# Kernel tuning notes

Measured on AMD Instinct MI355X. Metric: run time of the kernel, lower is better.

The kernel has to match this reference:

```python
import jax, jax.numpy as jnp
import numpy as np

H, HKV, DH = 32, 8, 128
ROPE_BASE = 500000.0


def _rope(x, pos):
    # x: [B, H, T, D]; MLX non-traditional rope (split halves)
    D = x.shape[-1]
    half = D // 2
    freqs = ROPE_BASE ** (-(jnp.arange(half, dtype=jnp.float32) * 2.0 / D))  # [half]
    t = pos + jnp.arange(x.shape[2], dtype=jnp.float32)                      # [T]
    ang = t[:, None] * freqs[None, :]                                        # [T, half]
    cos, sin = jnp.cos(ang), jnp.sin(ang)
    x1, x2 = x[..., :half], x[..., half:]
    return jnp.concatenate([x1 * cos - x2 * sin, x1 * sin + x2 * cos], axis=-1)


def setup_inputs() -> dict:
    key = jax.random.key(0)
    ks = jax.random.split(key, 5)
    B, T, HID = 1, 2048, 4096
    s = 0.02
    return {
        "hidden_states": jax.random.normal(ks[0], (B, T, HID), jnp.float32),
        "Wq": jax.random.normal(ks[1], (H * DH, HID), jnp.float32) * s,
        "Wk": jax.random.normal(ks[2], (HKV * DH, HID), jnp.float32) * s,
        "Wv": jax.random.normal(ks[3], (HKV * DH, HID), jnp.float32) * s,
        "Wo": jax.random.normal(ks[4], (HID, H * DH), jnp.float32) * s,
        "k_cache": jnp.zeros((1, HKV, 4096, DH), jnp.float32),
        "v_cache": jnp.zeros((1, HKV, 4096, DH), jnp.float32),
        "pos_int": 0,
    }


def reference(hidden_states, Wq, Wk, Wv, Wo, k_cache, v_cache, pos_int):
    B, T, _ = hidden_states.shape
    # QKV projections (no bias, Llama-style) -> [B, h, T, D]
    q = (hidden_states @ Wq.T).reshape(B, T, H, DH).transpose(0, 2, 1, 3)
    k = (hidden_states @ Wk.T).reshape(B, T, HKV, DH).transpose(0, 2, 1, 3)
    v = (hidden_states @ Wv.T).reshape(B, T, HKV, DH).transpose(0, 2, 1, 3)
    # RoPE with position offset
    q = _rope(q, pos_int)
    k = _rope(k, pos_int)
    # KV-cache scatter update at pos_int, then window to [:pos_int+T]
    k_cache = jax.lax.dynamic_update_slice(k_cache, k, (0, 0, pos_int, 0))
    v_cache = jax.lax.dynamic_update_slice(v_cache, v, (0, 0, pos_int, 0))
    Tk = pos_int + T
    k_win = k_cache[:, :, :Tk, :]
    v_win = v_cache[:, :, :Tk, :]
    # GQA: repeat_interleave KV heads to match query heads
    group = H // HKV
    k_ = jnp.repeat(k_win, group, axis=1)   # [B, H, Tk, D]
    v_ = jnp.repeat(v_win, group, axis=1)
    # SDPA, is_causal=True => top-left aligned causal mask (query i sees keys j<=i)
    scale = 1.0 / jnp.sqrt(jnp.asarray(DH, jnp.float32))
    scores = jnp.einsum("bhtd,bhsd->bhts", q, k_) * scale  # [B, H, T, Tk]
    causal = jnp.arange(Tk)[None, :] <= jnp.arange(T)[:, None]
    scores = jnp.where(causal[None, None], scores, jnp.finfo(scores.dtype).min)
    attn = jax.nn.softmax(scores, axis=-1)
    out = jnp.einsum("bhts,bhsd->bhtd", attn, v_)           # [B, H, T, D]
    out = out.transpose(0, 2, 1, 3).reshape(B, T, H * DH)
    return out @ Wo.T
```

## Files before the change

kernel.cpp:

```cpp
#include <hip/hip_runtime.h>


#define DEVI __device__ __forceinline__

typedef __attribute__((ext_vector_type(8))) short short8;
typedef __attribute__((ext_vector_type(4))) float f32x4;

DEVI unsigned short f2bf(float f) {
  union { float f; unsigned u; } x; x.f = f;
  unsigned r = x.u + 0x7FFFu + ((x.u >> 16) & 1u);
  return (unsigned short)(r >> 16);
}
DEVI float bf2f(unsigned short h) {
  union { unsigned u; float f; } x; x.u = ((unsigned)h) << 16;
  return x.f;
}
DEVI f32x4 mfma16(short8 a, short8 b, f32x4 c) {
  return __builtin_amdgcn_mfma_f32_16x16x32_bf16(a, b, c, 0, 0, 0);
}
DEVI void gl2lds16(const unsigned short* g, unsigned short* l) {
  __builtin_amdgcn_global_load_lds(
      (const __attribute__((address_space(1))) unsigned int*)g,
      (__attribute__((address_space(3))) unsigned int*)l, 16, 0, 0);
}
DEVI void bar() { __builtin_amdgcn_s_barrier(); }
DEVI void sfence() { __builtin_amdgcn_sched_barrier(0); }

DEVI void cvt_region(const float* __restrict__ src,
                     unsigned short* __restrict__ dst, int n4, int start,
                     int stride) {
  for (int i = start; i < n4; i += stride) {
    float4 v = ((const float4*)src)[i];
    ushort4 h;
    h.x = f2bf(v.x); h.y = f2bf(v.y); h.z = f2bf(v.z); h.w = f2bf(v.w);
    ((ushort4*)dst)[i] = h;
  }
}
__global__ __launch_bounds__(256)
void cvt5_kernel(const float* __restrict__ s0, const float* __restrict__ s1,
                 const float* __restrict__ s2, const float* __restrict__ s3,
                 const float* __restrict__ s4,
                 unsigned short* __restrict__ d0, unsigned short* __restrict__ d1,
                 unsigned short* __restrict__ d2, unsigned short* __restrict__ d3,
                 unsigned short* __restrict__ d4,
                 int n0, int n1, int n2, int n3, int n4) {
  const int start = blockIdx.x * 256 + threadIdx.x;
  const int stride = gridDim.x * 256;
  cvt_region(s0, d0, n0, start, stride);
  cvt_region(s1, d1, n1, start, stride);
  cvt_region(s2, d2, n2, start, stride);
  cvt_region(s3, d3, n3, start, stride);
  cvt_region(s4, d4, n4, start, stride);
}

__global__ __launch_bounds__(512, 2)
void gemm_qkv_8ph(const unsigned short* __restrict__ hsb,
                  const unsigned short* __restrict__ Wqb,
                  const unsigned short* __restrict__ Wkb,
                  const unsigned short* __restrict__ Wvb,
                  unsigned short* __restrict__ Qb,
                  unsigned short* __restrict__ Kb,
                  unsigned short* __restrict__ Vb) {
  const int K = 4096;
  const int NT = 64;
  __shared__ __align__(16) unsigned short Ls[2][2][2][256][32];
  const int tid = threadIdx.x, lane = tid & 63, w = tid >> 6;
  const int wr = w >> 2, wc = w & 3;
  const int bid = blockIdx.x;
  const int m0 = (bid & 7) * 256;
  const int n0g = (bid >> 3) * 256;

  const unsigned short* Bsrc; unsigned short* outp; int ldo, oc;
  if (n0g < 4096)      { Bsrc = Wqb + (size_t)n0g * K;          outp = Qb; ldo = 4096; oc = n0g; }
  else if (n0g < 5120) { Bsrc = Wkb + (size_t)(n0g - 4096) * K; outp = Kb; ldo = 1024; oc = n0g - 4096; }
  else                 { Bsrc = Wvb + (size_t)(n0g - 5120) * K; outp = Vb; ldo = 1024; oc = n0g - 5120; }
  const unsigned short* Asrc = hsb + (size_t)m0 * K;

  auto stageU = [&](const unsigned short* src, int ab, int kh, int tt, int bb) {
#pragma unroll
    for (int j = 0; j < 2; ++j) {
      const int seg = j * 8 + w;
      const int row = seg * 16 + (lane >> 2);
      const int cs  = (lane & 3) ^ ((row >> 1) & 3);
      gl2lds16(src + (size_t)row * K + tt * 64 + kh * 32 + cs * 8,
               &Ls[bb][ab][kh][seg * 16][0]);
    }
  };
  auto ldA = [&](int bb, int kh, int fm) -> short8 {
    const int ra = wr * 128 + fm * 16 + (lane & 15);
    const int cs = (lane >> 4) ^ ((ra >> 1) & 3);
    return *(const short8*)&Ls[bb][0][kh][ra][cs * 8];
  };
  auto ldB = [&](int bb, int kh, int fn) -> short8 {
    const int rb = wc * 64 + fn * 16 + (lane & 15);
    const int cs = (lane >> 4) ^ ((rb >> 1) & 3);
    return *(const short8*)&Ls[bb][1][kh][rb][cs * 8];
  };

  f32x4 acc[8][4];
#pragma unroll
  for (int i = 0; i < 8; ++i)
#pragma unroll
    for (int j = 0; j < 4; ++j) acc[i][j] = (f32x4){0.f, 0.f, 0.f, 0.f};

  stageU(Asrc, 0, 0, 0, 0);
  stageU(Asrc, 0, 1, 0, 0);
  stageU(Bsrc, 1, 0, 0, 0);
  stageU(Bsrc, 1, 1, 0, 0);
  stageU(Bsrc, 1, 0, 1, 1);
  stageU(Asrc, 0, 0, 1, 1);
  stageU(Bsrc, 1, 1, 1, 1);
  asm volatile("s_waitcnt vmcnt(6)" ::: "memory");
  bar();
  sfence();

  short8 af[4], bfr[4];
  for (int t = 0; t < NT; ++t) {
    const int bb = t & 1, nb = bb ^ 1;
#pragma unroll
    for (int i = 0; i < 4; ++i) af[i] = ldA(bb, 0, i);
#pragma unroll
    for (int i = 0; i < 4; ++i) bfr[i] = ldB(bb, 0, i);
    if (t + 1 < NT) stageU(Asrc, 0, 1, t + 1, nb);
    bar();
    __builtin_amdgcn_s_setprio(1);
#pragma unroll
    for (int i = 0; i < 4; ++i)
#pragma unroll
      for (int j = 0; j < 4; ++j) acc[i][j] = mfma16(af[i], bfr[j], acc[i][j]);
    __builtin_amdgcn_s_setprio(0);
    sfence(); bar(); sfence();
#pragma unroll
    for (int i = 0; i < 4; ++i) af[i] = ldA(bb, 0, 4 + i);
    if (t + 2 < NT) stageU(Bsrc, 1, 0, t + 2, bb);
    bar();
    __builtin_amdgcn_s_setprio(1);
#pragma unroll
    for (int i = 0; i < 4; ++i)
#pragma unroll
      for (int j = 0; j < 4; ++j) acc[4 + i][j] = mfma16(af[i], bfr[j], acc[4 + i][j]);
    __builtin_amdgcn_s_setprio(0);
    sfence(); bar(); sfence();
#pragma unroll
    for (int i = 0; i < 4; ++i) af[i] = ldA(bb, 1, i);
#pragma unroll
    for (int i = 0; i < 4; ++i) bfr[i] = ldB(bb, 1, i);
    if (t + 2 < NT) stageU(Asrc, 0, 0, t + 2, bb);
    bar();
    __builtin_amdgcn_s_setprio(1);
#pragma unroll
    for (int i = 0; i < 4; ++i)
#pragma unroll
      for (int j = 0; j < 4; ++j) acc[i][j] = mfma16(af[i], bfr[j], acc[i][j]);
    __builtin_amdgcn_s_setprio(0);
    sfence(); bar(); sfence();
#pragma unroll
    for (int i = 0; i < 4; ++i) af[i] = ldA(bb, 1, 4 + i);
    if (t + 2 < NT) stageU(Bsrc, 1, 1, t + 2, bb);
    bar();
    __builtin_amdgcn_s_setprio(1);
#pragma unroll
    for (int i = 0; i < 4; ++i)
#pragma unroll
      for (int j = 0; j < 4; ++j) acc[4 + i][j] = mfma16(af[i], bfr[j], acc[4 + i][j]);
    __builtin_amdgcn_s_setprio(0);
    if (t < NT - 2) asm volatile("s_waitcnt vmcnt(6)" ::: "memory");
    else            asm volatile("s_waitcnt vmcnt(0)" ::: "memory");
    sfence(); bar(); sfence();
  }

#pragma unroll
  for (int fm = 0; fm < 8; ++fm) {
    const int rb0 = m0 + wr * 128 + fm * 16 + ((lane >> 4) << 2);
#pragma unroll
    for (int fn = 0; fn < 4; ++fn) {
      const int cb = oc + wc * 64 + fn * 16 + (lane & 15);
#pragma unroll
      for (int r = 0; r < 4; ++r)
        outp[(size_t)(rb0 + r) * ldo + cb] = f2bf(acc[fm][fn][r]);
    }
  }
}

__global__ __launch_bounds__(256)
void postproc_kernel(const unsigned short* __restrict__ Vb,
                     unsigned short* __restrict__ VtG,
                     unsigned short* __restrict__ Qb,
                     unsigned short* __restrict__ Kb,
                     const int* __restrict__ posp) {
  __shared__ unsigned short tile[64][68];
  const int b = blockIdx.x, tid = threadIdx.x;
  if (b < 512) {
    const int t0 = (b & 31) * 64;
    const int c0 = (b >> 5) * 64;
    const int r = tid >> 4;
    const int c4 = (tid & 15) << 2;
#pragma unroll
    for (int i = 0; i < 4; ++i) {
      ushort4 v = *(const ushort4*)(Vb + (size_t)(t0 + r + i * 16) * 1024 + c0 + c4);
      *(ushort4*)&tile[r + i * 16][c4] = v;
    }
    __syncthreads();
#pragma unroll
    for (int i = 0; i < 4; ++i) {
      int d = r + i * 16;
      ushort4 o;
      o.x = tile[c4 + 0][d]; o.y = tile[c4 + 1][d];
      o.z = tile[c4 + 2][d]; o.w = tile[c4 + 3][d];
      *(ushort4*)(VtG + (size_t)(c0 + d) * 2048 + t0 + c4) = o;
    }
    return;
  }
  const int QP = 2048 * 32 * 64;
  const int KP = 2048 * 8 * 64;
  int idx = (b - 512) * 256 + tid;
  if (idx >= QP + KP) return;
  unsigned short* base; int t, hh, d, ld;
  if (idx < QP) {
    base = Qb; ld = 4096;
    t = idx >> 11; int rem = idx & 2047; hh = rem >> 6; d = rem & 63;
  } else {
    int j = idx - QP; base = Kb; ld = 1024;
    t = j >> 9; int rem = j & 511; hh = rem >> 6; d = rem & 63;
  }
  float freq = exp2f(-(float)d * 0.29580575880077f);
  float ang = (float)(t + posp[0]) * freq;
  float s, c;
  __sincosf(ang, &s, &c);
  size_t i1 = (size_t)t * ld + hh * 128 + d;
  float x1 = bf2f(base[i1]), x2 = bf2f(base[i1 + 64]);
  base[i1]      = f2bf(x1 * c - x2 * s);
  base[i1 + 64] = f2bf(x1 * s + x2 * c);
}

__global__ __launch_bounds__(512)
void attn_kernel(const unsigned short* __restrict__ Qb,
                 const unsigned short* __restrict__ Kb,
                 const unsigned short* __restrict__ VtG,
                 unsigned short* __restrict__ Ob) {
  __shared__ __align__(16) unsigned short Ks[2][64][128];
  __shared__ __align__(16) unsigned short Vt[2][128][64];
  __shared__ __align__(16) unsigned short Ps[8][16][64];
  const int tid = threadIdx.x, lane = tid & 63, w = tid >> 6;
  const int b = blockIdx.x;
  const int kh = b & 7;
  const int h  = kh * 4 + ((b >> 3) & 3);
  const int qi = b >> 5;
  const int qt = (qi < 8) ? qi : 23 - qi;
  const int q0 = qt * 128;
  const float SCALE = 0.08838834764831845f;

  short8 aq[4];
  {
    const int qrow = q0 + w * 16 + (lane & 15);
#pragma unroll
    for (int ks = 0; ks < 4; ++ks)
      aq[ks] = *(const short8*)(Qb + (size_t)qrow * 4096 + h * 128 + ks * 32 +
                                ((lane >> 4) << 3));
  }

  f32x4 o_acc[8];
#pragma unroll
  for (int n8 = 0; n8 < 8; ++n8) o_acc[n8] = (f32x4){0.f, 0.f, 0.f, 0.f};
  float mst[4], lst[4];
#pragma unroll
  for (int r = 0; r < 4; ++r) { mst[r] = -1e30f; lst[r] = 0.f; }

  auto stage = [&](int st, int bb) {
    const int s0 = st * 64;
#pragma unroll
    for (int j = 0; j < 2; ++j) {
      int sr = w * 8 + j * 4 + (lane >> 4);
      int sc = (((lane & 15) << 4) ^ ((sr & 7) << 4)) >> 1;
      gl2lds16(Kb + (size_t)(s0 + sr) * 1024 + kh * 128 + sc,
               &Ks[bb][w * 8 + j * 4][0]);
    }
#pragma unroll
    for (int j = 0; j < 2; ++j) {
      int dr = w * 16 + j * 8 + (lane >> 3);
      int sc = (((lane & 7) << 4) ^ ((dr & 7) << 4)) >> 1;
      gl2lds16(VtG + (size_t)(kh * 128 + dr) * 2048 + s0 + sc,
               &Vt[bb][w * 16 + j * 8][0]);
    }
  };

  const int ntiles = 2 * (qt + 1);
  stage(0, 0);
  for (int st = 0; st < ntiles; ++st) {
    const int cb = st & 1;
    const int s0 = st * 64;
    if (st + 1 < ntiles) {
      stage(st + 1, cb ^ 1);
      asm volatile("s_waitcnt vmcnt(4)" ::: "memory");
    } else {
      asm volatile("s_waitcnt vmcnt(0)" ::: "memory");
    }
    bar(); sfence();

    f32x4 sacc[4];
#pragma unroll
    for (int ni = 0; ni < 4; ++ni) sacc[ni] = (f32x4){0.f, 0.f, 0.f, 0.f};
#pragma unroll
    for (int ks = 0; ks < 4; ++ks) {
      const int co = ks * 64 + ((lane >> 4) << 4);
      short8 bk[4];
#pragma unroll
      for (int ni = 0; ni < 4; ++ni) {
        int kr = ni * 16 + (lane & 15);
        bk[ni] = *(const short8*)((const char*)(&Ks[cb][kr][0]) + (co ^ ((kr & 7) << 4)));
      }
#pragma unroll
      for (int ni = 0; ni < 4; ++ni)
        sacc[ni] = mfma16(aq[ks], bk[ni], sacc[ni]);
    }

    char* pb = (char*)(&Ps[w][0][0]);
#pragma unroll
    for (int r = 0; r < 4; ++r) {
      const int qrow = q0 + w * 16 + ((lane >> 4) << 2) + r;
      float v4[4]; float vmax = -1e30f;
#pragma unroll
      for (int ni = 0; ni < 4; ++ni) {
        int scol = s0 + ni * 16 + (lane & 15);
        float x = sacc[ni][r] * SCALE;
        if (scol > qrow) x = -1e30f;
        v4[ni] = x; vmax = fmaxf(vmax, x);
      }
      vmax = fmaxf(vmax, __shfl_xor(vmax, 1));
      vmax = fmaxf(vmax, __shfl_xor(vmax, 2));
      vmax = fmaxf(vmax, __shfl_xor(vmax, 4));
      vmax = fmaxf(vmax, __shfl_xor(vmax, 8));
      float mo = mst[r];
      float mn = fmaxf(mo, vmax);
      float al = __expf(mo - mn);
      float rs = 0.f;
      const int prow = ((lane >> 4) << 2) + r;
      const int pswz = ((prow >> 2) & 3) << 5;
#pragma unroll
      for (int ni = 0; ni < 4; ++ni) {
        float p = __expf(v4[ni] - mn);
        rs += p;
        int cbyte = (ni * 16 + (lane & 15)) * 2;
        *(unsigned short*)(pb + prow * 128 + (cbyte ^ pswz)) = f2bf(p);
      }
      rs += __shfl_xor(rs, 1);
      rs += __shfl_xor(rs, 2);
      rs += __shfl_xor(rs, 4);
      rs += __shfl_xor(rs, 8);
      lst[r] = lst[r] * al + rs;
      mst[r] = mn;
#pragma unroll
      for (int n8 = 0; n8 < 8; ++n8) o_acc[n8][r] *= al;
    }

#pragma unroll
    for (int ks2 = 0; ks2 < 2; ++ks2) {
      const int co = ks2 * 64 + ((lane >> 4) << 4);
      const int pr = lane & 15;
      short8 pa = *(const short8*)(pb + pr * 128 + (co ^ (((pr >> 2) & 3) << 5)));
#pragma unroll
      for (int n8 = 0; n8 < 8; ++n8) {
        int vr = n8 * 16 + (lane & 15);
        short8 bv = *(const short8*)((const char*)(&Vt[cb][vr][0]) + (co ^ ((vr & 7) << 4)));
        o_acc[n8] = mfma16(pa, bv, o_acc[n8]);
      }
    }
    sfence(); bar(); sfence();
  }

#pragma unroll
  for (int r = 0; r < 4; ++r) {
    float inv = 1.0f / lst[r];
    int row = q0 + w * 16 + ((lane >> 4) << 2) + r;
#pragma unroll
    for (int n8 = 0; n8 < 8; ++n8)
      Ob[(size_t)row * 4096 + h * 128 + n8 * 16 + (lane & 15)] =
          f2bf(o_acc[n8][r] * inv);
  }
}

__global__ __launch_bounds__(256, 2)
void gemm_out_bf16(const unsigned short* __restrict__ Ab,
                   const unsigned short* __restrict__ Wob,
                   float* __restrict__ Cout) {
  const int K = 4096;
  __shared__ __align__(16) unsigned short As[128][64];
  __shared__ __align__(16) unsigned short Bs[128][64];
  const int tid = threadIdx.x, lane = tid & 63, wid = tid >> 6;
  const int bid = blockIdx.x;
  const int m0 = (((bid & 7) + 8 * (bid >> 8))) * 128;
  const int n0 = ((bid >> 3) & 31) * 128;
  const unsigned short* Asrc = Ab + (size_t)m0 * K;
  const unsigned short* Bsrc = Wob + (size_t)n0 * K;

  f32x4 acc[4][4];
#pragma unroll
  for (int i = 0; i < 4; ++i)
#pragma unroll
    for (int j = 0; j < 4; ++j) acc[i][j] = (f32x4){0.f, 0.f, 0.f, 0.f};

  const int wm = (wid >> 1) * 64, wn = (wid & 1) * 64;
  const int srow = wid * 32 + (lane >> 3);
  const int scol = (lane & 7) * 8;

  for (int k0 = 0; k0 < K; k0 += 64) {
#pragma unroll
    for (int i = 0; i < 4; ++i) {
      gl2lds16(Asrc + (size_t)(srow + i * 8) * K + k0 + scol, &As[wid * 32 + i * 8][0]);
      gl2lds16(Bsrc + (size_t)(srow + i * 8) * K + k0 + scol, &Bs[wid * 32 + i * 8][0]);
    }
    __syncthreads();
#pragma unroll
    for (int ks = 0; ks < 2; ++ks) {
      short8 af[4], bfr[4];
      const int co = ks * 64 + ((lane >> 4) << 4);
#pragma unroll
      for (int i = 0; i < 4; ++i) {
        af[i]  = *(const short8*)((const char*)(&As[wm + i * 16 + (lane & 15)][0]) + co);
        bfr[i] = *(const short8*)((const char*)(&Bs[wn + i * 16 + (lane & 15)][0]) + co);
      }
#pragma unroll
      for (int i = 0; i < 4; ++i)
#pragma unroll
        for (int j = 0; j < 4; ++j)
          acc[i][j] = mfma16(af[i], bfr[j], acc[i][j]);
    }
    __syncthreads();
  }

#pragma unroll
  for (int i = 0; i < 4; ++i) {
    int rb = m0 + wm + i * 16 + ((lane >> 4) << 2);
#pragma unroll
    for (int j = 0; j < 4; ++j) {
      int cb = n0 + wn + j * 16 + (lane & 15);
#pragma unroll
      for (int r = 0; r < 4; ++r)
        Cout[(size_t)(rb + r) * 4096 + cb] = acc[i][j][r];
    }
  }
}

extern "C" void kernel_launch(void* const* d_in, const int* in_sizes, int n_in,
                              void* d_out, int out_size, void* d_ws, size_t ws_size,
                              hipStream_t stream) {
  const float* hs = (const float*)d_in[0];
  const float* Wq = (const float*)d_in[1];
  const float* Wk = (const float*)d_in[2];
  const float* Wv = (const float*)d_in[3];
  const float* Wo = (const float*)d_in[4];
  const int* pos = (const int*)d_in[7];

  unsigned short* hsb = (unsigned short*)d_ws;
  unsigned short* Wqb = hsb + (size_t)8  * 1024 * 1024;
  unsigned short* Wkb = Wqb + (size_t)16 * 1024 * 1024;
  unsigned short* Wvb = Wkb + (size_t)4  * 1024 * 1024;
  unsigned short* Wob = Wvb + (size_t)4  * 1024 * 1024;
  unsigned short* Qb  = Wob + (size_t)16 * 1024 * 1024;
  unsigned short* Kb  = Qb  + (size_t)8  * 1024 * 1024;
  unsigned short* Vb  = Kb  + (size_t)2  * 1024 * 1024;
  unsigned short* Ob  = Vb  + (size_t)2  * 1024 * 1024;
  unsigned short* VtG = hsb;
  float* out = (float*)d_out;

  cvt5_kernel<<<dim3(2048), 256, 0, stream>>>(
      hs, Wq, Wk, Wv, Wo, hsb, Wqb, Wkb, Wvb, Wob,
      2 * 1024 * 1024, 4 * 1024 * 1024, 1 * 1024 * 1024, 1 * 1024 * 1024,
      4 * 1024 * 1024);

  gemm_qkv_8ph<<<dim3(192), 512, 0, stream>>>(hsb, Wqb, Wkb, Wvb, Qb, Kb, Vb);

  const int npairs = 2048 * 32 * 64 + 2048 * 8 * 64;
  const int rope_blocks = (npairs + 255) / 256;
  postproc_kernel<<<dim3(512 + rope_blocks), 256, 0, stream>>>(Vb, VtG, Qb, Kb, pos);

  attn_kernel<<<dim3(512), 512, 0, stream>>>(Qb, Kb, VtG, Ob);
  gemm_out_bf16<<<dim3(512), 256, 0, stream>>>(Ob, Wob, out);
}
```

Baseline: 359.7 us.

## Pipeline output GEMM, add lazy softmax rescale, remap QKV grid to 2D

The output projection GEMM is replaced by a 512-thread, 256x128-tile kernel. It double-buffers global-to-LDS loads in half-K phases with swizzled LDS and raises wave priority around the MFMA blocks, to overlap memory traffic with compute. The attention softmax now rescales the running max and accumulators only when some lane's new max exceeds the old one by more than a threshold, which skips most of the per-tile rescale multiplies. The QKV GEMM block index is moved to a 2D grid, which changes the order blocks are dispatched in and so their cache reuse. The lazy rescale lets exponentials exceed 1 by up to e^8 before renormalizing, which may affect bf16 precision of P.

```diff
diff --git a/kernel.cpp b/kernel.cpp
--- a/kernel.cpp
+++ b/kernel.cpp
@@ -66,9 +66,8 @@
   __shared__ __align__(16) unsigned short Ls[2][2][2][256][32];
   const int tid = threadIdx.x, lane = tid & 63, w = tid >> 6;
   const int wr = w >> 2, wc = w & 3;
-  const int bid = blockIdx.x;
-  const int m0 = (bid & 7) * 256;
-  const int n0g = (bid >> 3) * 256;
+  const int m0 = blockIdx.y * 256;
+  const int n0g = blockIdx.x * 256;
 
   const unsigned short* Bsrc; unsigned short* outp; int ldo, oc;
   if (n0g < 4096)      { Bsrc = Wqb + (size_t)n0g * K;          outp = Qb; ldo = 4096; oc = n0g; }
@@ -331,14 +330,21 @@
       vmax = fmaxf(vmax, __shfl_xor(vmax, 4));
       vmax = fmaxf(vmax, __shfl_xor(vmax, 8));
       float mo = mst[r];
-      float mn = fmaxf(mo, vmax);
-      float al = __expf(mo - mn);
+      if (!__all(vmax <= mo + 8.0f)) {
+        float mn = fmaxf(mo, vmax);
+        float al = __expf(mo - mn);
+        lst[r] *= al;
+#pragma unroll
+        for (int n8 = 0; n8 < 8; ++n8) o_acc[n8][r] *= al;
+        mst[r] = mn;
+      }
+      float m_use = mst[r];
       float rs = 0.f;
       const int prow = ((lane >> 4) << 2) + r;
       const int pswz = ((prow >> 2) & 3) << 5;
 #pragma unroll
       for (int ni = 0; ni < 4; ++ni) {
-        float p = __expf(v4[ni] - mn);
+        float p = __expf(v4[ni] - m_use);
         rs += p;
         int cbyte = (ni * 16 + (lane & 15)) * 2;
         *(unsigned short*)(pb + prow * 128 + (cbyte ^ pswz)) = f2bf(p);
@@ -347,10 +353,7 @@
       rs += __shfl_xor(rs, 2);
       rs += __shfl_xor(rs, 4);
       rs += __shfl_xor(rs, 8);
-      lst[r] = lst[r] * al + rs;
-      mst[r] = mn;
-#pragma unroll
-      for (int n8 = 0; n8 < 8; ++n8) o_acc[n8][r] *= al;
+      lst[r] += rs;
     }
 
 #pragma unroll
@@ -379,64 +382,130 @@
   }
 }
 
-__global__ __launch_bounds__(256, 2)
-void gemm_out_bf16(const unsigned short* __restrict__ Ab,
-                   const unsigned short* __restrict__ Wob,
-                   float* __restrict__ Cout) {
+__global__ __launch_bounds__(512, 2)
+void gemm_out_8ph(const unsigned short* __restrict__ Ab,
+                  const unsigned short* __restrict__ Wob,
+                  float* __restrict__ Cout) {
   const int K = 4096;
-  __shared__ __align__(16) unsigned short As[128][64];
-  __shared__ __align__(16) unsigned short Bs[128][64];
-  const int tid = threadIdx.x, lane = tid & 63, wid = tid >> 6;
+  const int NT = 64;
+  __shared__ __align__(16) unsigned short LA[2][2][256][32];
+  __shared__ __align__(16) unsigned short LB[2][2][128][32];
+  const int tid = threadIdx.x, lane = tid & 63, w = tid >> 6;
+  const int wr = w >> 1, wc = w & 1;
   const int bid = blockIdx.x;
-  const int m0 = (((bid & 7) + 8 * (bid >> 8))) * 128;
-  const int n0 = ((bid >> 3) & 31) * 128;
+  const int m0 = (bid >> 5) * 256;
+  const int n0 = (bid & 31) * 128;
   const unsigned short* Asrc = Ab + (size_t)m0 * K;
   const unsigned short* Bsrc = Wob + (size_t)n0 * K;
 
+  auto stageA = [&](int kh, int tt, int bb) {
+#pragma unroll
+    for (int j = 0; j < 2; ++j) {
+      const int seg = j * 8 + w;
+      const int row = seg * 16 + (lane >> 2);
+      const int cs  = (lane & 3) ^ ((row >> 1) & 3);
+      gl2lds16(Asrc + (size_t)row * K + tt * 64 + kh * 32 + cs * 8,
+               &LA[bb][kh][seg * 16][0]);
+    }
+  };
+  auto stageB = [&](int kh, int tt, int bb) {
+    const int row = w * 16 + (lane >> 2);
+    const int cs  = (lane & 3) ^ ((row >> 1) & 3);
+    gl2lds16(Bsrc + (size_t)row * K + tt * 64 + kh * 32 + cs * 8,
+             &LB[bb][kh][w * 16][0]);
+  };
+  auto ldA = [&](int bb, int kh, int fm) -> short8 {
+    const int ra = wr * 64 + fm * 16 + (lane & 15);
+    const int cs = (lane >> 4) ^ ((ra >> 1) & 3);
+    return *(const short8*)&LA[bb][kh][ra][cs * 8];
+  };
+  auto ldB = [&](int bb, int kh, int fn) -> short8 {
+    const int rb = wc * 64 + fn * 16 + (lane & 15);
+    const int cs = (lane >> 4) ^ ((rb >> 1) & 3);
+    return *(const short8*)&LB[bb][kh][rb][cs * 8];
+  };
+
   f32x4 acc[4][4];
 #pragma unroll
   for (int i = 0; i < 4; ++i)
 #pragma unroll
     for (int j = 0; j < 4; ++j) acc[i][j] = (f32x4){0.f, 0.f, 0.f, 0.f};
 
-  const int wm = (wid >> 1) * 64, wn = (wid & 1) * 64;
-  const int srow = wid * 32 + (lane >> 3);
-  const int scol = (lane & 7) * 8;
-
-  for (int k0 = 0; k0 < K; k0 += 64) {
-#pragma unroll
-    for (int i = 0; i < 4; ++i) {
-      gl2lds16(Asrc + (size_t)(srow + i * 8) * K + k0 + scol, &As[wid * 32 + i * 8][0]);
-      gl2lds16(Bsrc + (size_t)(srow + i * 8) * K + k0 + scol, &Bs[wid * 32 + i * 8][0]);
-    }
-    __syncthreads();
-#pragma unroll
-    for (int ks = 0; ks < 2; ++ks) {
-      short8 af[4], bfr[4];
-      const int co = ks * 64 + ((lane >> 4) << 4);
-#pragma unroll
-      for (int i = 0; i < 4; ++i) {
-        af[i]  = *(const short8*)((const char*)(&As[wm + i * 16 + (lane & 15)][0]) + co);
-        bfr[i] = *(const short8*)((const char*)(&Bs[wn + i * 16 + (lane & 15)][0]) + co);
-      }
-#pragma unroll
-      for (int i = 0; i < 4; ++i)
-#pragma unroll
-        for (int j = 0; j < 4; ++j)
-          acc[i][j] = mfma16(af[i], bfr[j], acc[i][j]);
-    }
-    __syncthreads();
-  }
-
-#pragma unroll
-  for (int i = 0; i < 4; ++i) {
-    int rb = m0 + wm + i * 16 + ((lane >> 4) << 2);
-#pragma unroll
-    for (int j = 0; j < 4; ++j) {
-      int cb = n0 + wn + j * 16 + (lane & 15);
+  stageA(0, 0, 0);
+  stageA(1, 0, 0);
+  stageB(0, 0, 0);
+  stageB(1, 0, 0);
+  stageB(0, 1, 1);
+  stageA(0, 1, 1);
+  stageB(1, 1, 1);
+  asm volatile("s_waitcnt vmcnt(4)" ::: "memory");
+  bar();
+  sfence();
+
+  short8 af[2], bfr[4];
+  for (int t = 0; t < NT; ++t) {
+    const int bb = t & 1, nb = bb ^ 1;
+#pragma unroll
+    for (int i = 0; i < 2; ++i) af[i] = ldA(bb, 0, i);
+#pragma unroll
+    for (int i = 0; i < 4; ++i) bfr[i] = ldB(bb, 0, i);
+    if (t + 1 < NT) stageA(1, t + 1, nb);
+    bar();
+    __builtin_amdgcn_s_setprio(1);
+#pragma unroll
+    for (int i = 0; i < 2; ++i)
+#pragma unroll
+      for (int j = 0; j < 4; ++j) acc[i][j] = mfma16(af[i], bfr[j], acc[i][j]);
+    __builtin_amdgcn_s_setprio(0);
+    sfence(); bar(); sfence();
+#pragma unroll
+    for (int i = 0; i < 2; ++i) af[i] = ldA(bb, 0, 2 + i);
+    if (t + 2 < NT) stageB(0, t + 2, bb);
+    bar();
+    __builtin_amdgcn_s_setprio(1);
+#pragma unroll
+    for (int i = 0; i < 2; ++i)
+#pragma unroll
+      for (int j = 0; j < 4; ++j) acc[2 + i][j] = mfma16(af[i], bfr[j], acc[2 + i][j]);
+    __builtin_amdgcn_s_setprio(0);
+    sfence(); bar(); sfence();
+#pragma unroll
+    for (int i = 0; i < 2; ++i) af[i] = ldA(bb, 1, i);
+#pragma unroll
+    for (int i = 0; i < 4; ++i) bfr[i] = ldB(bb, 1, i);
+    if (t + 2 < NT) stageA(0, t + 2, bb);
+    bar();
+    __builtin_amdgcn_s_setprio(1);
+#pragma unroll
+    for (int i = 0; i < 2; ++i)
+#pragma unroll
+      for (int j = 0; j < 4; ++j) acc[i][j] = mfma16(af[i], bfr[j], acc[i][j]);
+    __builtin_amdgcn_s_setprio(0);
+    sfence(); bar(); sfence();
+#pragma unroll
+    for (int i = 0; i < 2; ++i) af[i] = ldA(bb, 1, 2 + i);
+    if (t + 2 < NT) stageB(1, t + 2, bb);
+    bar();
+    __builtin_amdgcn_s_setprio(1);
+#pragma unroll
+    for (int i = 0; i < 2; ++i)
+#pragma unroll
+      for (int j = 0; j < 4; ++j) acc[2 + i][j] = mfma16(af[i], bfr[j], acc[2 + i][j]);
+    __builtin_amdgcn_s_setprio(0);
+    if (t < NT - 2) asm volatile("s_waitcnt vmcnt(4)" ::: "memory");
+    else            asm volatile("s_waitcnt vmcnt(0)" ::: "memory");
+    sfence(); bar(); sfence();
+  }
+
+#pragma unroll
+  for (int fm = 0; fm < 4; ++fm) {
+    const int rb0 = m0 + wr * 64 + fm * 16 + ((lane >> 4) << 2);
+#pragma unroll
+    for (int fn = 0; fn < 4; ++fn) {
+      const int cb = n0 + wc * 64 + fn * 16 + (lane & 15);
 #pragma unroll
       for (int r = 0; r < 4; ++r)
-        Cout[(size_t)(rb + r) * 4096 + cb] = acc[i][j][r];
+        Cout[(size_t)(rb0 + r) * 4096 + cb] = acc[fm][fn][r];
     }
   }
 }
@@ -468,12 +537,12 @@
       2 * 1024 * 1024, 4 * 1024 * 1024, 1 * 1024 * 1024, 1 * 1024 * 1024,
       4 * 1024 * 1024);
 
-  gemm_qkv_8ph<<<dim3(192), 512, 0, stream>>>(hsb, Wqb, Wkb, Wvb, Qb, Kb, Vb);
+  gemm_qkv_8ph<<<dim3(24, 8), 512, 0, stream>>>(hsb, Wqb, Wkb, Wvb, Qb, Kb, Vb);
 
   const int npairs = 2048 * 32 * 64 + 2048 * 8 * 64;
   const int rope_blocks = (npairs + 255) / 256;
   postproc_kernel<<<dim3(512 + rope_blocks), 256, 0, stream>>>(Vb, VtG, Qb, Kb, pos);
 
   attn_kernel<<<dim3(512), 512, 0, stream>>>(Qb, Kb, VtG, Ob);
-  gemm_out_bf16<<<dim3(512), 256, 0, stream>>>(Ob, Wob, out);
-}
+  gemm_out_8ph<<<dim3(256), 512, 0, stream>>>(Ob, Wob, out);
+}
```

Result: no change. 366.4 us (+1.9%).
